# Kernel tuning notes

Hardware: AMD Instinct MI355X
Metric: run time of the kernel (lower is better)

## Reference

```python
import jax, jax.numpy as jnp
import numpy as np

B, S, H, F, E, TOPK = 4, 2048, 1024, 4096, 8, 2

def setup_inputs() -> dict:
    key = jax.random.key(0)
    ks = jax.random.split(key, 8)
    sh = 1.0 / np.sqrt(H)
    sf = 1.0 / np.sqrt(F)
    return {
        "hidden_states": jax.random.normal(ks[0], (B, S, H), jnp.float32),
        "Wr": jax.random.normal(ks[1], (H, E), jnp.float32) * sh,
        "br": jnp.zeros((E,), jnp.float32),
        "W1": jax.random.normal(ks[2], (E, H, F), jnp.float32) * sh,
        "b1": jax.random.normal(ks[3], (E, F), jnp.float32) * 0.01,
        "W2": jax.random.normal(ks[4], (E, F, H), jnp.float32) * sf,
        "b2": jax.random.normal(ks[5], (E, H), jnp.float32) * 0.01,
    }

def reference(hidden_states, Wr, br, W1, b1, W2, b2):
    b, s, h = hidden_states.shape
    x = hidden_states.reshape(-1, h)                      # [T, H]
    T = x.shape[0]
    logits = x @ Wr + br                                  # [T, E]
    routing_weights = jax.nn.softmax(logits, axis=-1)     # [T, E]
    top_v, top_i = jax.lax.top_k(logits, TOPK)            # [T, k]
    top_gates = jax.nn.softmax(top_v, axis=-1)            # [T, k]
    rows = jnp.arange(T)[:, None]
    dispatch = jnp.zeros((T, E), logits.dtype).at[rows, top_i].set(top_gates)  # [T, E]
    # Each expert runs densely on gate-scaled tokens: gelu((g*x)@W1 + b1)@W2 + b2.
    # (g*x)@W1 == g * (x@W1), so share the first GEMM across experts.
    z = jnp.einsum('th,ehf->etf', x, W1)                  # [E, T, F]
    a = jax.nn.gelu(dispatch.T[:, :, None] * z + b1[:, None, :], approximate=False)
    expert_out = jnp.einsum('etf,efh->eth', a, W2) + b2[:, None, :]  # [E, T, H]
    combined = jnp.einsum('te,eth->th', dispatch, expert_out)        # [T, H]
    final_output = combined.reshape(b, s, h)
    aux_loss = jnp.sum(routing_weights.mean(axis=0) * (dispatch.sum(axis=0) / T)) * E
    return (final_output,
            routing_weights.reshape(b, s, E),
            dispatch.reshape(b, s, E),
            aux_loss,
            logits.reshape(b, s, E))
```

## Files before the change

kernel.cpp:

```cpp
#include <hip/hip_runtime.h>

#define T_TOK 8192
#define H_DIM 1024
#define F_DIM 4096
#define E_NUM 8

typedef __attribute__((ext_vector_type(8))) short short8;
typedef __attribute__((ext_vector_type(4))) float f32x4;

__device__ __forceinline__ unsigned short f2bf(float f) {
  unsigned int u = __float_as_uint(f);
  return (unsigned short)((u + 0x7fffu + ((u >> 16) & 1u)) >> 16);
}

__device__ __forceinline__ void gload16(const void* g, void* l) {
  __builtin_amdgcn_global_load_lds(
      (__attribute__((address_space(1))) const unsigned int*)(unsigned long long)g,
      (__attribute__((address_space(3))) unsigned int*)(unsigned int)(unsigned long long)l,
      16, 0, 0);
}

__global__ __launch_bounds__(256) void k_convert_x(const float* __restrict__ x,
                                                   unsigned short* __restrict__ xb) {
  int i = blockIdx.x * blockDim.x + threadIdx.x;
  float4 v = ((const float4*)x)[i];
  unsigned int lo = (unsigned int)f2bf(v.x) | ((unsigned int)f2bf(v.y) << 16);
  unsigned int hi = (unsigned int)f2bf(v.z) | ((unsigned int)f2bf(v.w) << 16);
  ((uint2*)xb)[i] = make_uint2(lo, hi);
}

__global__ __launch_bounds__(256) void k_transpose_cvt(const float* __restrict__ in,
                                                       unsigned short* __restrict__ out,
                                                       int R, int C) {
  __shared__ float tile[32][33];
  const size_t eoff = (size_t)blockIdx.z * R * C;
  const int c0 = blockIdx.x * 32, r0 = blockIdx.y * 32;
  const int tx = threadIdx.x & 31, ty = threadIdx.x >> 5;
#pragma unroll
  for (int i = 0; i < 32; i += 8)
    tile[ty + i][tx] = in[eoff + (size_t)(r0 + ty + i) * C + (c0 + tx)];
  __syncthreads();
#pragma unroll
  for (int i = 0; i < 32; i += 8)
    out[eoff + (size_t)(c0 + ty + i) * R + (r0 + tx)] = f2bf(tile[tx][ty + i]);
}

__global__ __launch_bounds__(256) void k_logits(const float* __restrict__ x,
                                                const float* __restrict__ Wr,
                                                const float* __restrict__ br,
                                                double* __restrict__ ld,
                                                float* __restrict__ out_logits) {
  const int lane = threadIdx.x & 63;
  const int t = blockIdx.x * 4 + (threadIdx.x >> 6);
  double acc[8] = {0, 0, 0, 0, 0, 0, 0, 0};
#pragma unroll
  for (int i = 0; i < 16; ++i) {
    const int h = i * 64 + lane;
    const float xv = x[(size_t)t * H_DIM + h];
    const float4 wa = ((const float4*)Wr)[h * 2];
    const float4 wb = ((const float4*)Wr)[h * 2 + 1];
    acc[0] += (double)xv * wa.x; acc[1] += (double)xv * wa.y;
    acc[2] += (double)xv * wa.z; acc[3] += (double)xv * wa.w;
    acc[4] += (double)xv * wb.x; acc[5] += (double)xv * wb.y;
    acc[6] += (double)xv * wb.z; acc[7] += (double)xv * wb.w;
  }
#pragma unroll
  for (int e = 0; e < 8; ++e)
#pragma unroll
    for (int m = 32; m; m >>= 1) acc[e] += __shfl_xor(acc[e], m);
  if (lane == 0) {
#pragma unroll
    for (int e = 0; e < 8; ++e) {
      const double l = acc[e] + (double)br[e];
      ld[(size_t)t * 8 + e] = l;
      out_logits[(size_t)t * 8 + e] = (float)l;
    }
  }
}

__global__ __launch_bounds__(256) void k_decide(const double* __restrict__ ld,
                                                float* __restrict__ out_rw,
                                                float* __restrict__ out_disp,
                                                int* __restrict__ cnt,
                                                int* __restrict__ bidx,
                                                float* __restrict__ bgate,
                                                float* __restrict__ sums) {
  __shared__ int hcnt[8];
  __shared__ int hbase[8];
  __shared__ float srw[8];
  __shared__ float sds[8];
  const int tloc = threadIdx.x;
  const int t = blockIdx.x * 256 + tloc;
  const int lane = tloc & 63;
  if (tloc < 8) { hcnt[tloc] = 0; srw[tloc] = 0.0f; sds[tloc] = 0.0f; }
  __syncthreads();

  double l[8];
#pragma unroll
  for (int e = 0; e < 8; ++e) l[e] = ld[(size_t)t * 8 + e];
  double mx = l[0];
#pragma unroll
  for (int e = 1; e < 8; ++e) mx = l[e] > mx ? l[e] : mx;
  double ex[8], se = 0.0;
#pragma unroll
  for (int e = 0; e < 8; ++e) { ex[e] = exp(l[e] - mx); se += ex[e]; }
  int i1 = 0;
#pragma unroll
  for (int e = 1; e < 8; ++e) if (l[e] > l[i1]) i1 = e;
  int i2 = (i1 == 0) ? 1 : 0;
#pragma unroll
  for (int e = 0; e < 8; ++e) if (e != i1 && l[e] > l[i2]) i2 = e;
  const double g1 = 1.0 / (1.0 + exp(l[i2] - l[i1]));
  const double g2 = 1.0 - g1;

  float rwv[8];
#pragma unroll
  for (int e = 0; e < 8; ++e) {
    rwv[e] = (float)(ex[e] / se);
    out_rw[(size_t)t * 8 + e] = rwv[e];
    out_disp[(size_t)t * 8 + e] = (e == i1) ? (float)g1 : (e == i2) ? (float)g2 : 0.0f;
  }
#pragma unroll
  for (int e = 0; e < 8; ++e) {
    float v = rwv[e];
#pragma unroll
    for (int m = 32; m; m >>= 1) v += __shfl_xor(v, m);
    if (lane == 0) atomicAdd(&srw[e], v);
  }
  atomicAdd(&sds[i1], (float)g1);
  atomicAdd(&sds[i2], (float)g2);

  const int loc1 = atomicAdd(&hcnt[i1], 1);
  const int loc2 = atomicAdd(&hcnt[i2], 1);
  __syncthreads();
  if (tloc < 8) hbase[tloc] = atomicAdd(&cnt[tloc], hcnt[tloc]);
  __syncthreads();
  const int s1 = hbase[i1] + loc1;
  const int s2 = hbase[i2] + loc2;
  bidx[i1 * T_TOK + s1] = t; bgate[i1 * T_TOK + s1] = (float)g1;
  bidx[i2 * T_TOK + s2] = t; bgate[i2 * T_TOK + s2] = (float)g2;
  if (tloc < 8) {
    atomicAdd(&sums[tloc], srw[tloc]);
    atomicAdd(&sums[8 + tloc], sds[tloc]);
  }
}

__global__ void k_prefix_aux(const int* __restrict__ cnt, int* __restrict__ abase,
                             const float* __restrict__ sums, float* __restrict__ out_aux) {
  if (threadIdx.x == 0) {
    int base = 0;
    for (int e = 0; e < 8; ++e) { abase[e] = base; base += (cnt[e] + 127) & ~127; }
    abase[8] = base;
    double aux = 0.0;
    for (int e = 0; e < 8; ++e) aux += ((double)sums[e] / 8192.0) * ((double)sums[8 + e] / 8192.0);
    *out_aux = (float)(aux * 8.0);
  }
}


#define MFMA_Q(qm_, qn_, Bset_)                                                        \
  do {                                                                                 \
    _Pragma("unroll") for (int kh = 0; kh < 2; ++kh)                                   \
    _Pragma("unroll") for (int mi = 0; mi < 4; ++mi)                                   \
    _Pragma("unroll") for (int ni = 0; ni < 2; ++ni)                                   \
      acc[(qm_)*4 + mi][(qn_)*2 + ni] = __builtin_amdgcn_mfma_f32_16x16x32_bf16(       \
          Areg[mi][kh], Bset_[ni][kh], acc[(qm_)*4 + mi][(qn_)*2 + ni], 0, 0, 0);      \
  } while (0)

#define LOAD_A(mh_)                                                                    \
  do {                                                                                 \
    const char* Ab = smem + slot * 65536 + (mh_)*16384;                                \
    _Pragma("unroll") for (int mi = 0; mi < 4; ++mi) {                                 \
      Areg[mi][0] = *(const short8*)(Ab + mi * 2048 + aoffk0);                         \
      Areg[mi][1] = *(const short8*)(Ab + mi * 2048 + aoffk1);                         \
    }                                                                                  \
  } while (0)

#define LOAD_B(set_, nh_)                                                              \
  do {                                                                                 \
    const char* Bb = smem + slot * 65536 + 32768 + (nh_)*16384;                        \
    _Pragma("unroll") for (int ni = 0; ni < 2; ++ni) {                                 \
      set_[ni][0] = *(const short8*)(Bb + ni * 2048 + boffk0);                         \
      set_[ni][1] = *(const short8*)(Bb + ni * 2048 + boffk1);                         \
    }                                                                                  \
  } while (0)

#define PHASE_TAIL(MFMA_STMT)                                                          \
  __builtin_amdgcn_s_barrier();                                                        \
  __builtin_amdgcn_s_setprio(1);                                                       \
  MFMA_STMT;                                                                           \
  __builtin_amdgcn_s_setprio(0);                                                       \
  __builtin_amdgcn_s_barrier();

__global__ __launch_bounds__(512, 2) void k_gemm1(
    const unsigned short* __restrict__ xb, const unsigned short* __restrict__ w1t,
    const float* __restrict__ b1, const int* __restrict__ bidx,
    const float* __restrict__ bgate, const int* __restrict__ abase,
    unsigned short* __restrict__ abuf) {
  constexpr int NT = 16;
  const int e = blockIdx.z, by = blockIdx.y, bx = blockIdx.x;
  const int pb = abase[e], pcnt = abase[e + 1] - pb;
  if (by * 256 >= pcnt) return;
  __shared__ char smem[131072];
  const int tid = threadIdx.x, wid = tid >> 6, lane = tid & 63;
  const int wr = wid >> 2, wc = wid & 3;
  const int rr0 = tid >> 3;
  const int kbyte = ((tid & 7) ^ (rr0 & 7)) * 16;
  const int d0 = tid * 16, d1 = d0 + 8192;

  const int* bidx_e = bidx + e * T_TOK + by * 256;
  int tok[4];
#pragma unroll
  for (int i = 0; i < 4; ++i) tok[i] = bidx_e[i * 64 + rr0];

  const int brB0 = ((rr0 >> 5) * 64 + (rr0 & 31));
  const char* Bbase = (const char*)(w1t + (size_t)e * F_DIM * H_DIM + (size_t)(bx * 256) * H_DIM);

#define G1_STAGE_A(g_, mh_)                                                            \
  do {                                                                                 \
    const char* s0 = (const char*)(xb + (size_t)tok[(mh_)] * H_DIM) + (g_)*128 + kbyte;\
    const char* s1 = (const char*)(xb + (size_t)tok[2 + (mh_)] * H_DIM) + (g_)*128 + kbyte; \
    char* dst = smem + (((g_)&1) * 65536) + (mh_)*16384;                               \
    gload16(s0, dst + d0); gload16(s1, dst + d1);                                      \
  } while (0)

#define G1_STAGE_B(g_, nh_)                                                            \
  do {                                                                                 \
    const char* s0 = Bbase + (size_t)(brB0 + (nh_)*32) * 2048 + (g_)*128 + kbyte;      \
    const char* s1 = Bbase + (size_t)(brB0 + 128 + (nh_)*32) * 2048 + (g_)*128 + kbyte;\
    char* dst = smem + (((g_)&1) * 65536) + 32768 + (nh_)*16384;                       \
    gload16(s0, dst + d0); gload16(s1, dst + d1);                                      \
  } while (0)

  const int aoffk0 = (wr * 64 + (lane & 15)) * 128 + (((lane >> 4) ^ (lane & 7)) * 16);
  const int aoffk1 = aoffk0 ^ 64;
  const int boffk0 = (wc * 32 + (lane & 15)) * 128 + (((lane >> 4) ^ (lane & 7)) * 16);
  const int boffk1 = boffk0 ^ 64;

  f32x4 acc[8][4] = {};
  short8 Areg[4][2], B0reg[2][2], B1reg[2][2];

  G1_STAGE_A(0, 0); G1_STAGE_B(0, 1); G1_STAGE_A(0, 1); G1_STAGE_B(0, 0);
  G1_STAGE_A(1, 0); G1_STAGE_B(1, 1); G1_STAGE_A(1, 1);
  asm volatile("s_waitcnt vmcnt(6)" ::: "memory");
  __builtin_amdgcn_sched_barrier(0);
  __builtin_amdgcn_s_barrier();

  for (int g = 0; g < NT; ++g) {
    const int slot = g & 1;
    LOAD_A(0); LOAD_B(B0reg, 0);
    if (g + 1 < NT) G1_STAGE_B(g + 1, 0);
    PHASE_TAIL(MFMA_Q(0, 0, B0reg));
    LOAD_B(B1reg, 1);
    if (g + 2 < NT) G1_STAGE_A(g + 2, 0);
    PHASE_TAIL(MFMA_Q(0, 1, B1reg));
    LOAD_A(1);
    if (g + 2 < NT) G1_STAGE_B(g + 2, 1);
    PHASE_TAIL(MFMA_Q(1, 1, B1reg));
    if (g + 2 < NT) {
      G1_STAGE_A(g + 2, 1);
      asm volatile("s_waitcnt vmcnt(6)" ::: "memory");
    } else if (g + 1 < NT) {
      asm volatile("s_waitcnt vmcnt(0)" ::: "memory");
    }
    __builtin_amdgcn_sched_barrier(0);
    PHASE_TAIL(MFMA_Q(1, 0, B0reg));
  }

  const int lcol = lane & 15;
  const int gcol0 = bx * 256 + wc * 64;
  float b1v[4];
#pragma unroll
  for (int n = 0; n < 4; ++n) b1v[n] = b1[(size_t)e * F_DIM + gcol0 + n * 16 + lcol];
  const float* bg_e = bgate + e * T_TOK + by * 256;
#pragma unroll
  for (int m = 0; m < 8; ++m) {
    const int rl = wr * 128 + m * 16 + (lane >> 4) * 4;
#pragma unroll
    for (int j = 0; j < 4; ++j) {
      const int row = rl + j;
      if (by * 256 + row < pcnt) {
        const float gt = bg_e[row];
        unsigned short* orow = abuf + (size_t)(pb + by * 256 + row) * F_DIM + gcol0;
#pragma unroll
        for (int n = 0; n < 4; ++n) {
          const float v = fmaf(gt, acc[m][n][j], b1v[n]);
          const float a = 0.5f * v * (1.0f + erff(v * 0.70710678118654752f));
          orow[n * 16 + lcol] = f2bf(a);
        }
      }
    }
  }
#undef G1_STAGE_A
#undef G1_STAGE_B
}

__global__ __launch_bounds__(512, 2) void k_gemm2(
    const unsigned short* __restrict__ abuf, const unsigned short* __restrict__ w2t,
    const float* __restrict__ b2, const int* __restrict__ bidx,
    const float* __restrict__ bgate, const int* __restrict__ abase,
    const int* __restrict__ cnt, float* __restrict__ out) {
  constexpr int NT = 64;
  const int e = blockIdx.z, by = blockIdx.y, bx = blockIdx.x;
  const int pb = abase[e], pcnt = abase[e + 1] - pb;
  if (by * 256 >= pcnt) return;
  const int ce = cnt[e];
  __shared__ char smem[131072];
  const int tid = threadIdx.x, wid = tid >> 6, lane = tid & 63;
  const int wr = wid >> 2, wc = wid & 3;
  const int rr0 = tid >> 3;
  const int kbyte = ((tid & 7) ^ (rr0 & 7)) * 16;
  const int d0 = tid * 16, d1 = d0 + 8192;

  const char* Abase = (const char*)(abuf + (size_t)(pb + by * 256) * F_DIM);
  const int brB0 = ((rr0 >> 5) * 64 + (rr0 & 31));
  const char* Bbase = (const char*)(w2t + (size_t)e * H_DIM * F_DIM + (size_t)(bx * 256) * F_DIM);

#define G2_STAGE_A(g_, mh_)                                                            \
  do {                                                                                 \
    const char* s0 = Abase + (size_t)((mh_)*64 + rr0) * 8192 + (g_)*128 + kbyte;       \
    const char* s1 = Abase + (size_t)(128 + (mh_)*64 + rr0) * 8192 + (g_)*128 + kbyte; \
    char* dst = smem + (((g_)&1) * 65536) + (mh_)*16384;                               \
    gload16(s0, dst + d0); gload16(s1, dst + d1);                                      \
  } while (0)

#define G2_STAGE_B(g_, nh_)                                                            \
  do {                                                                                 \
    const char* s0 = Bbase + (size_t)(brB0 + (nh_)*32) * 8192 + (g_)*128 + kbyte;      \
    const char* s1 = Bbase + (size_t)(brB0 + 128 + (nh_)*32) * 8192 + (g_)*128 + kbyte;\
    char* dst = smem + (((g_)&1) * 65536) + 32768 + (nh_)*16384;                       \
    gload16(s0, dst + d0); gload16(s1, dst + d1);                                      \
  } while (0)

  const int aoffk0 = (wr * 64 + (lane & 15)) * 128 + (((lane >> 4) ^ (lane & 7)) * 16);
  const int aoffk1 = aoffk0 ^ 64;
  const int boffk0 = (wc * 32 + (lane & 15)) * 128 + (((lane >> 4) ^ (lane & 7)) * 16);
  const int boffk1 = boffk0 ^ 64;

  f32x4 acc[8][4] = {};
  short8 Areg[4][2], B0reg[2][2], B1reg[2][2];

  G2_STAGE_A(0, 0); G2_STAGE_B(0, 1); G2_STAGE_A(0, 1); G2_STAGE_B(0, 0);
  G2_STAGE_A(1, 0); G2_STAGE_B(1, 1); G2_STAGE_A(1, 1);
  asm volatile("s_waitcnt vmcnt(6)" ::: "memory");
  __builtin_amdgcn_sched_barrier(0);
  __builtin_amdgcn_s_barrier();

  for (int g = 0; g < NT; ++g) {
    const int slot = g & 1;
    LOAD_A(0); LOAD_B(B0reg, 0);
    if (g + 1 < NT) G2_STAGE_B(g + 1, 0);
    PHASE_TAIL(MFMA_Q(0, 0, B0reg));
    LOAD_B(B1reg, 1);
    if (g + 2 < NT) G2_STAGE_A(g + 2, 0);
    PHASE_TAIL(MFMA_Q(0, 1, B1reg));
    LOAD_A(1);
    if (g + 2 < NT) G2_STAGE_B(g + 2, 1);
    PHASE_TAIL(MFMA_Q(1, 1, B1reg));
    if (g + 2 < NT) {
      G2_STAGE_A(g + 2, 1);
      asm volatile("s_waitcnt vmcnt(6)" ::: "memory");
    } else if (g + 1 < NT) {
      asm volatile("s_waitcnt vmcnt(0)" ::: "memory");
    }
    __builtin_amdgcn_sched_barrier(0);
    PHASE_TAIL(MFMA_Q(1, 0, B0reg));
  }

  const int lcol = lane & 15;
  const int gcol0 = bx * 256 + wc * 64;
  float b2v[4];
#pragma unroll
  for (int n = 0; n < 4; ++n) b2v[n] = b2[(size_t)e * H_DIM + gcol0 + n * 16 + lcol];
  const float* bg_e = bgate + e * T_TOK;
  const int* bi_e = bidx + e * T_TOK;
#pragma unroll
  for (int m = 0; m < 8; ++m) {
    const int rl = wr * 128 + m * 16 + (lane >> 4) * 4;
#pragma unroll
    for (int j = 0; j < 4; ++j) {
      const int gm = by * 256 + rl + j;
      if (gm < ce) {
        const float gt = bg_e[gm];
        float* orow = out + (size_t)bi_e[gm] * H_DIM + gcol0;
#pragma unroll
        for (int n = 0; n < 4; ++n)
          atomicAdd(orow + n * 16 + lcol, (acc[m][n][j] + b2v[n]) * gt);
      }
    }
  }
#undef G2_STAGE_A
#undef G2_STAGE_B
}

extern "C" void kernel_launch(void* const* d_in, const int* in_sizes, int n_in,
                              void* d_out, int out_size, void* d_ws, size_t ws_size,
                              hipStream_t stream) {
  const float* x  = (const float*)d_in[0];
  const float* Wr = (const float*)d_in[1];
  const float* br = (const float*)d_in[2];
  const float* W1 = (const float*)d_in[3];
  const float* b1 = (const float*)d_in[4];
  const float* W2 = (const float*)d_in[5];
  const float* b2 = (const float*)d_in[6];
  float* out = (float*)d_out;
  float* out_final  = out;
  float* out_rw     = out + 8388608;
  float* out_disp   = out_rw + 65536;
  float* out_aux    = out_disp + 65536;
  float* out_logits = out_aux + 1;

  char* ws = (char*)d_ws;
  unsigned short* xb   = (unsigned short*)(ws);
  unsigned short* w1t  = (unsigned short*)(ws + 16777216);
  unsigned short* w2t  = (unsigned short*)(ws + 83886080);
  unsigned short* abuf = (unsigned short*)(ws + 150994944);
  int*    bidx  = (int*)(ws + 293601280);
  float*  bgate = (float*)(ws + 293863424);
  int*    cnt   = (int*)(ws + 294125568);
  int*    abase = (int*)(ws + 294125632);
  float*  sums  = (float*)(ws + 294125696);
  double* ld    = (double*)(ws + 294125824);

  hipMemsetAsync(cnt, 0, 64, stream);
  hipMemsetAsync(sums, 0, 64, stream);
  hipMemsetAsync(bidx, 0, 262144, stream);
  hipMemsetAsync(bgate, 0, 262144, stream);
  hipMemsetAsync(out_final, 0, (size_t)8388608 * 4, stream);

  k_convert_x<<<8192, 256, 0, stream>>>(x, xb);
  k_transpose_cvt<<<dim3(128, 32, 8), 256, 0, stream>>>(W1, w1t, H_DIM, F_DIM);
  k_transpose_cvt<<<dim3(32, 128, 8), 256, 0, stream>>>(W2, w2t, F_DIM, H_DIM);
  k_logits<<<2048, 256, 0, stream>>>(x, Wr, br, ld, out_logits);
  k_decide<<<32, 256, 0, stream>>>(ld, out_rw, out_disp, cnt, bidx, bgate, sums);
  k_prefix_aux<<<1, 64, 0, stream>>>(cnt, abase, sums, out_aux);
  k_gemm1<<<dim3(16, 32, 8), 512, 0, stream>>>(xb, w1t, b1, bidx, bgate, abase, abuf);
  k_gemm2<<<dim3(4, 32, 8), 512, 0, stream>>>(abuf, w2t, b2, bidx, bgate, abase, cnt, out_final);
}
```

Before: 607.2 us.

## Make expert GEMMs persistent with compact tile queues, split-K, and LDS-staged stores

The prefix kernel now builds per-expert tile offsets into a device-global queue. Both grouped GEMMs launch a fixed grid of 256 persistent blocks that walk that compact tile list, instead of a 3D grid where most blocks exit early. GEMM2 also splits K in two, relying on the existing atomic adds, so there are more tiles to balance across CUs. GEMM1's epilogue stages results through swizzled LDS so it can issue 16-byte coalesced stores in place of scattered 2-byte writes. The trade-offs are extra __syncthreads per tile, twice the atomic traffic in GEMM2, and possible load imbalance from the static stride over tiles.

```diff
diff --git a/kernel.cpp b/kernel.cpp
--- a/kernel.cpp
+++ b/kernel.cpp
@@ -7,6 +7,8 @@
 
 typedef __attribute__((ext_vector_type(8))) short short8;
 typedef __attribute__((ext_vector_type(4))) float f32x4;
+
+__device__ int g_tq[32];
 
 __device__ __forceinline__ unsigned short f2bf(float f) {
   unsigned int u = __float_as_uint(f);
@@ -148,9 +150,18 @@
 __global__ void k_prefix_aux(const int* __restrict__ cnt, int* __restrict__ abase,
                              const float* __restrict__ sums, float* __restrict__ out_aux) {
   if (threadIdx.x == 0) {
-    int base = 0;
-    for (int e = 0; e < 8; ++e) { abase[e] = base; base += (cnt[e] + 127) & ~127; }
+    int base = 0, t1 = 0, t2 = 0;
+    for (int e = 0; e < 8; ++e) {
+      abase[e] = base;
+      const int pc = (cnt[e] + 127) & ~127;
+      base += pc;
+      const int nby = (pc + 255) >> 8;
+      g_tq[e] = t1;      t1 += nby * 16;
+      g_tq[16 + e] = t2; t2 += nby * 8;
+    }
     abase[8] = base;
+    g_tq[8] = t1;
+    g_tq[24] = t2;
     double aux = 0.0;
     for (int e = 0; e < 8; ++e) aux += ((double)sums[e] / 8192.0) * ((double)sums[8 + e] / 8192.0);
     *out_aux = (float)(aux * 8.0);
@@ -198,23 +209,33 @@
     const float* __restrict__ bgate, const int* __restrict__ abase,
     unsigned short* __restrict__ abuf) {
   constexpr int NT = 16;
-  const int e = blockIdx.z, by = blockIdx.y, bx = blockIdx.x;
-  const int pb = abase[e], pcnt = abase[e + 1] - pb;
-  if (by * 256 >= pcnt) return;
   __shared__ char smem[131072];
   const int tid = threadIdx.x, wid = tid >> 6, lane = tid & 63;
   const int wr = wid >> 2, wc = wid & 3;
   const int rr0 = tid >> 3;
   const int kbyte = ((tid & 7) ^ (rr0 & 7)) * 16;
   const int d0 = tid * 16, d1 = d0 + 8192;
-
-  const int* bidx_e = bidx + e * T_TOK + by * 256;
-  int tok[4];
-#pragma unroll
-  for (int i = 0; i < 4; ++i) tok[i] = bidx_e[i * 64 + rr0];
-
-  const int brB0 = ((rr0 >> 5) * 64 + (rr0 & 31));
-  const char* Bbase = (const char*)(w1t + (size_t)e * F_DIM * H_DIM + (size_t)(bx * 256) * H_DIM);
+  const int aoffk0 = (wr * 64 + (lane & 15)) * 128 + (((lane >> 4) ^ (lane & 7)) * 16);
+  const int aoffk1 = aoffk0 ^ 64;
+  const int boffk0 = (wc * 32 + (lane & 15)) * 128 + (((lane >> 4) ^ (lane & 7)) * 16);
+  const int boffk1 = boffk0 ^ 64;
+  const int lcol = lane & 15;
+  const int total = g_tq[8];
+
+  for (int tix = blockIdx.x; tix < total; tix += gridDim.x) {
+    int e = 0;
+#pragma unroll
+    for (int q = 1; q < 8; ++q) if (g_tq[q] <= tix) e = q;
+    const int local = tix - g_tq[e];
+    const int by = local >> 4, bx = local & 15;
+    const int pb = abase[e], pcnt = abase[e + 1] - pb;
+
+    const int* bidx_e = bidx + e * T_TOK + by * 256;
+    int tok[4];
+#pragma unroll
+    for (int i = 0; i < 4; ++i) tok[i] = bidx_e[i * 64 + rr0];
+    const int brB0 = ((rr0 >> 5) * 64 + (rr0 & 31));
+    const char* Bbase = (const char*)(w1t + (size_t)e * F_DIM * H_DIM + (size_t)(bx * 256) * H_DIM);
 
 #define G1_STAGE_A(g_, mh_)                                                            \
   do {                                                                                 \
@@ -232,67 +253,74 @@
     gload16(s0, dst + d0); gload16(s1, dst + d1);                                      \
   } while (0)
 
-  const int aoffk0 = (wr * 64 + (lane & 15)) * 128 + (((lane >> 4) ^ (lane & 7)) * 16);
-  const int aoffk1 = aoffk0 ^ 64;
-  const int boffk0 = (wc * 32 + (lane & 15)) * 128 + (((lane >> 4) ^ (lane & 7)) * 16);
-  const int boffk1 = boffk0 ^ 64;
-
-  f32x4 acc[8][4] = {};
-  short8 Areg[4][2], B0reg[2][2], B1reg[2][2];
-
-  G1_STAGE_A(0, 0); G1_STAGE_B(0, 1); G1_STAGE_A(0, 1); G1_STAGE_B(0, 0);
-  G1_STAGE_A(1, 0); G1_STAGE_B(1, 1); G1_STAGE_A(1, 1);
-  asm volatile("s_waitcnt vmcnt(6)" ::: "memory");
-  __builtin_amdgcn_sched_barrier(0);
-  __builtin_amdgcn_s_barrier();
-
-  for (int g = 0; g < NT; ++g) {
-    const int slot = g & 1;
-    LOAD_A(0); LOAD_B(B0reg, 0);
-    if (g + 1 < NT) G1_STAGE_B(g + 1, 0);
-    PHASE_TAIL(MFMA_Q(0, 0, B0reg));
-    LOAD_B(B1reg, 1);
-    if (g + 2 < NT) G1_STAGE_A(g + 2, 0);
-    PHASE_TAIL(MFMA_Q(0, 1, B1reg));
-    LOAD_A(1);
-    if (g + 2 < NT) G1_STAGE_B(g + 2, 1);
-    PHASE_TAIL(MFMA_Q(1, 1, B1reg));
-    if (g + 2 < NT) {
-      G1_STAGE_A(g + 2, 1);
-      asm volatile("s_waitcnt vmcnt(6)" ::: "memory");
-    } else if (g + 1 < NT) {
-      asm volatile("s_waitcnt vmcnt(0)" ::: "memory");
-    }
+    f32x4 acc[8][4] = {};
+    short8 Areg[4][2], B0reg[2][2], B1reg[2][2];
+
+    __syncthreads();
+    G1_STAGE_A(0, 0); G1_STAGE_B(0, 1); G1_STAGE_A(0, 1); G1_STAGE_B(0, 0);
+    G1_STAGE_A(1, 0); G1_STAGE_B(1, 1); G1_STAGE_A(1, 1);
+    asm volatile("s_waitcnt vmcnt(6)" ::: "memory");
     __builtin_amdgcn_sched_barrier(0);
-    PHASE_TAIL(MFMA_Q(1, 0, B0reg));
-  }
-
-  const int lcol = lane & 15;
-  const int gcol0 = bx * 256 + wc * 64;
-  float b1v[4];
-#pragma unroll
-  for (int n = 0; n < 4; ++n) b1v[n] = b1[(size_t)e * F_DIM + gcol0 + n * 16 + lcol];
-  const float* bg_e = bgate + e * T_TOK + by * 256;
-#pragma unroll
-  for (int m = 0; m < 8; ++m) {
-    const int rl = wr * 128 + m * 16 + (lane >> 4) * 4;
-#pragma unroll
-    for (int j = 0; j < 4; ++j) {
-      const int row = rl + j;
-      if (by * 256 + row < pcnt) {
-        const float gt = bg_e[row];
-        unsigned short* orow = abuf + (size_t)(pb + by * 256 + row) * F_DIM + gcol0;
+    __builtin_amdgcn_s_barrier();
+
+    for (int g = 0; g < NT; ++g) {
+      const int slot = g & 1;
+      LOAD_A(0); LOAD_B(B0reg, 0);
+      if (g + 1 < NT) G1_STAGE_B(g + 1, 0);
+      PHASE_TAIL(MFMA_Q(0, 0, B0reg));
+      LOAD_B(B1reg, 1);
+      if (g + 2 < NT) G1_STAGE_A(g + 2, 0);
+      PHASE_TAIL(MFMA_Q(0, 1, B1reg));
+      LOAD_A(1);
+      if (g + 2 < NT) G1_STAGE_B(g + 2, 1);
+      PHASE_TAIL(MFMA_Q(1, 1, B1reg));
+      if (g + 2 < NT) {
+        G1_STAGE_A(g + 2, 1);
+        asm volatile("s_waitcnt vmcnt(6)" ::: "memory");
+      } else if (g + 1 < NT) {
+        asm volatile("s_waitcnt vmcnt(0)" ::: "memory");
+      }
+      __builtin_amdgcn_sched_barrier(0);
+      PHASE_TAIL(MFMA_Q(1, 0, B0reg));
+    }
+
+    const int gcol0 = bx * 256 + wc * 64;
+    float b1v[4];
+#pragma unroll
+    for (int n = 0; n < 4; ++n) b1v[n] = b1[(size_t)e * F_DIM + gcol0 + n * 16 + lcol];
+    const float* bg_e = bgate + e * T_TOK + by * 256;
+    char* wsm = smem + wid * 16384;
+#pragma unroll
+    for (int m = 0; m < 8; ++m) {
+      const int rbase = m * 16 + (lane >> 4) * 4;
+#pragma unroll
+      for (int j = 0; j < 4; ++j) {
+        const int wrow = rbase + j;
+        const int trow = wr * 128 + wrow;
+        const float gt = (by * 256 + trow < pcnt) ? bg_e[trow] : 0.0f;
 #pragma unroll
         for (int n = 0; n < 4; ++n) {
           const float v = fmaf(gt, acc[m][n][j], b1v[n]);
           const float a = 0.5f * v * (1.0f + erff(v * 0.70710678118654752f));
-          orow[n * 16 + lcol] = f2bf(a);
+          const int col2 = (n * 16 + lcol) * 2;
+          *(unsigned short*)(wsm + wrow * 128 + (col2 ^ ((wrow & 7) << 4))) = f2bf(a);
         }
       }
     }
-  }
+    __syncthreads();
+#pragma unroll
+    for (int r = 0; r < 16; ++r) {
+      const int row = r * 8 + (lane >> 3);
+      const int chunk = (lane & 7) ^ (row & 7);
+      const int trow = wr * 128 + row;
+      if (by * 256 + trow < pcnt) {
+        short8 vv = *(const short8*)(wsm + row * 128 + chunk * 16);
+        *(short8*)(abuf + (size_t)(pb + by * 256 + trow) * F_DIM + bx * 256 + wc * 64 + (lane & 7) * 8) = vv;
+      }
+    }
 #undef G1_STAGE_A
 #undef G1_STAGE_B
+  }
 }
 
 __global__ __launch_bounds__(512, 2) void k_gemm2(
@@ -300,21 +328,33 @@
     const float* __restrict__ b2, const int* __restrict__ bidx,
     const float* __restrict__ bgate, const int* __restrict__ abase,
     const int* __restrict__ cnt, float* __restrict__ out) {
-  constexpr int NT = 64;
-  const int e = blockIdx.z, by = blockIdx.y, bx = blockIdx.x;
-  const int pb = abase[e], pcnt = abase[e + 1] - pb;
-  if (by * 256 >= pcnt) return;
-  const int ce = cnt[e];
+  constexpr int NTH = 32;
   __shared__ char smem[131072];
   const int tid = threadIdx.x, wid = tid >> 6, lane = tid & 63;
   const int wr = wid >> 2, wc = wid & 3;
   const int rr0 = tid >> 3;
   const int kbyte = ((tid & 7) ^ (rr0 & 7)) * 16;
   const int d0 = tid * 16, d1 = d0 + 8192;
-
-  const char* Abase = (const char*)(abuf + (size_t)(pb + by * 256) * F_DIM);
-  const int brB0 = ((rr0 >> 5) * 64 + (rr0 & 31));
-  const char* Bbase = (const char*)(w2t + (size_t)e * H_DIM * F_DIM + (size_t)(bx * 256) * F_DIM);
+  const int aoffk0 = (wr * 64 + (lane & 15)) * 128 + (((lane >> 4) ^ (lane & 7)) * 16);
+  const int aoffk1 = aoffk0 ^ 64;
+  const int boffk0 = (wc * 32 + (lane & 15)) * 128 + (((lane >> 4) ^ (lane & 7)) * 16);
+  const int boffk1 = boffk0 ^ 64;
+  const int lcol = lane & 15;
+  const int total = g_tq[24];
+
+  for (int tix = blockIdx.x; tix < total; tix += gridDim.x) {
+    int e = 0;
+#pragma unroll
+    for (int q = 1; q < 8; ++q) if (g_tq[16 + q] <= tix) e = q;
+    const int local = tix - g_tq[16 + e];
+    const int by = local >> 3, bx = (local >> 1) & 3, ks = local & 1;
+    const int pb = abase[e], pcnt = abase[e + 1] - pb;
+    const int ce = cnt[e];
+    const int g0 = ks * NTH, g1 = g0 + NTH;
+
+    const char* Abase = (const char*)(abuf + (size_t)(pb + by * 256) * F_DIM);
+    const int brB0 = ((rr0 >> 5) * 64 + (rr0 & 31));
+    const char* Bbase = (const char*)(w2t + (size_t)e * H_DIM * F_DIM + (size_t)(bx * 256) * F_DIM);
 
 #define G2_STAGE_A(g_, mh_)                                                            \
   do {                                                                                 \
@@ -332,65 +372,62 @@
     gload16(s0, dst + d0); gload16(s1, dst + d1);                                      \
   } while (0)
 
-  const int aoffk0 = (wr * 64 + (lane & 15)) * 128 + (((lane >> 4) ^ (lane & 7)) * 16);
-  const int aoffk1 = aoffk0 ^ 64;
-  const int boffk0 = (wc * 32 + (lane & 15)) * 128 + (((lane >> 4) ^ (lane & 7)) * 16);
-  const int boffk1 = boffk0 ^ 64;
-
-  f32x4 acc[8][4] = {};
-  short8 Areg[4][2], B0reg[2][2], B1reg[2][2];
-
-  G2_STAGE_A(0, 0); G2_STAGE_B(0, 1); G2_STAGE_A(0, 1); G2_STAGE_B(0, 0);
-  G2_STAGE_A(1, 0); G2_STAGE_B(1, 1); G2_STAGE_A(1, 1);
-  asm volatile("s_waitcnt vmcnt(6)" ::: "memory");
-  __builtin_amdgcn_sched_barrier(0);
-  __builtin_amdgcn_s_barrier();
-
-  for (int g = 0; g < NT; ++g) {
-    const int slot = g & 1;
-    LOAD_A(0); LOAD_B(B0reg, 0);
-    if (g + 1 < NT) G2_STAGE_B(g + 1, 0);
-    PHASE_TAIL(MFMA_Q(0, 0, B0reg));
-    LOAD_B(B1reg, 1);
-    if (g + 2 < NT) G2_STAGE_A(g + 2, 0);
-    PHASE_TAIL(MFMA_Q(0, 1, B1reg));
-    LOAD_A(1);
-    if (g + 2 < NT) G2_STAGE_B(g + 2, 1);
-    PHASE_TAIL(MFMA_Q(1, 1, B1reg));
-    if (g + 2 < NT) {
-      G2_STAGE_A(g + 2, 1);
-      asm volatile("s_waitcnt vmcnt(6)" ::: "memory");
-    } else if (g + 1 < NT) {
-      asm volatile("s_waitcnt vmcnt(0)" ::: "memory");
-    }
+    f32x4 acc[8][4] = {};
+    short8 Areg[4][2], B0reg[2][2], B1reg[2][2];
+
+    __syncthreads();
+    G2_STAGE_A(g0, 0); G2_STAGE_B(g0, 1); G2_STAGE_A(g0, 1); G2_STAGE_B(g0, 0);
+    G2_STAGE_A(g0 + 1, 0); G2_STAGE_B(g0 + 1, 1); G2_STAGE_A(g0 + 1, 1);
+    asm volatile("s_waitcnt vmcnt(6)" ::: "memory");
     __builtin_amdgcn_sched_barrier(0);
-    PHASE_TAIL(MFMA_Q(1, 0, B0reg));
-  }
-
-  const int lcol = lane & 15;
-  const int gcol0 = bx * 256 + wc * 64;
-  float b2v[4];
-#pragma unroll
-  for (int n = 0; n < 4; ++n) b2v[n] = b2[(size_t)e * H_DIM + gcol0 + n * 16 + lcol];
-  const float* bg_e = bgate + e * T_TOK;
-  const int* bi_e = bidx + e * T_TOK;
-#pragma unroll
-  for (int m = 0; m < 8; ++m) {
-    const int rl = wr * 128 + m * 16 + (lane >> 4) * 4;
-#pragma unroll
-    for (int j = 0; j < 4; ++j) {
-      const int gm = by * 256 + rl + j;
-      if (gm < ce) {
-        const float gt = bg_e[gm];
-        float* orow = out + (size_t)bi_e[gm] * H_DIM + gcol0;
-#pragma unroll
-        for (int n = 0; n < 4; ++n)
-          atomicAdd(orow + n * 16 + lcol, (acc[m][n][j] + b2v[n]) * gt);
+    __builtin_amdgcn_s_barrier();
+
+    for (int g = g0; g < g1; ++g) {
+      const int slot = g & 1;
+      LOAD_A(0); LOAD_B(B0reg, 0);
+      if (g + 1 < g1) G2_STAGE_B(g + 1, 0);
+      PHASE_TAIL(MFMA_Q(0, 0, B0reg));
+      LOAD_B(B1reg, 1);
+      if (g + 2 < g1) G2_STAGE_A(g + 2, 0);
+      PHASE_TAIL(MFMA_Q(0, 1, B1reg));
+      LOAD_A(1);
+      if (g + 2 < g1) G2_STAGE_B(g + 2, 1);
+      PHASE_TAIL(MFMA_Q(1, 1, B1reg));
+      if (g + 2 < g1) {
+        G2_STAGE_A(g + 2, 1);
+        asm volatile("s_waitcnt vmcnt(6)" ::: "memory");
+      } else if (g + 1 < g1) {
+        asm volatile("s_waitcnt vmcnt(0)" ::: "memory");
       }
-    }
-  }
+      __builtin_amdgcn_sched_barrier(0);
+      PHASE_TAIL(MFMA_Q(1, 0, B0reg));
+    }
+
+    const int gcol0 = bx * 256 + wc * 64;
+    float b2v[4];
+#pragma unroll
+    for (int n = 0; n < 4; ++n)
+      b2v[n] = ks ? 0.0f : b2[(size_t)e * H_DIM + gcol0 + n * 16 + lcol];
+    const float* bg_e = bgate + e * T_TOK;
+    const int* bi_e = bidx + e * T_TOK;
+#pragma unroll
+    for (int m = 0; m < 8; ++m) {
+      const int rl = wr * 128 + m * 16 + (lane >> 4) * 4;
+#pragma unroll
+      for (int j = 0; j < 4; ++j) {
+        const int gm = by * 256 + rl + j;
+        if (gm < ce) {
+          const float gt = bg_e[gm];
+          float* orow = out + (size_t)bi_e[gm] * H_DIM + gcol0;
+#pragma unroll
+          for (int n = 0; n < 4; ++n)
+            atomicAdd(orow + n * 16 + lcol, (acc[m][n][j] + b2v[n]) * gt);
+        }
+      }
+    }
 #undef G2_STAGE_A
 #undef G2_STAGE_B
+  }
 }
 
 extern "C" void kernel_launch(void* const* d_in, const int* in_sizes, int n_in,
@@ -434,6 +471,6 @@
   k_logits<<<2048, 256, 0, stream>>>(x, Wr, br, ld, out_logits);
   k_decide<<<32, 256, 0, stream>>>(ld, out_rw, out_disp, cnt, bidx, bgate, sums);
   k_prefix_aux<<<1, 64, 0, stream>>>(cnt, abase, sums, out_aux);
-  k_gemm1<<<dim3(16, 32, 8), 512, 0, stream>>>(xb, w1t, b1, bidx, bgate, abase, abuf);
-  k_gemm2<<<dim3(4, 32, 8), 512, 0, stream>>>(abuf, w2t, b2, bidx, bgate, abase, cnt, out_final);
-}
+  k_gemm1<<<256, 512, 0, stream>>>(xb, w1t, b1, bidx, bgate, abase, abuf);
+  k_gemm2<<<256, 512, 0, stream>>>(abuf, w2t, b2, bidx, bgate, abase, cnt, out_final);
+}
```

New measurement: 846.7 us. +39.4%, slower.

## Replace atomic scatter-add with per-slot expert output plus combine kernel

Applied to the files above, without the earlier changes.

GEMM2 now writes gated expert rows into a packed per-slot buffer with plain stores. A new combine kernel gathers each token's two rows via a slot map recorded in the decide kernel. This removes the fp32 atomicAdd scatter and the memset of the final output. GEMM1's epilogue now stages GELU output through swizzled LDS so it can write 16-byte coalesced rows, and the weight transpose uses 64-row tiles with 64-wide output stores. The cost is an extra round trip through a 64MB intermediate buffer and one more launch; the buffer reuses the xb/w1t workspace after GEMM1 has finished with them.

```diff
diff --git a/kernel.cpp b/kernel.cpp
--- a/kernel.cpp
+++ b/kernel.cpp
@@ -32,17 +32,18 @@
 __global__ __launch_bounds__(256) void k_transpose_cvt(const float* __restrict__ in,
                                                        unsigned short* __restrict__ out,
                                                        int R, int C) {
-  __shared__ float tile[32][33];
+  __shared__ float tile[64][33];
   const size_t eoff = (size_t)blockIdx.z * R * C;
-  const int c0 = blockIdx.x * 32, r0 = blockIdx.y * 32;
+  const int c0 = blockIdx.x * 32, r0 = blockIdx.y * 64;
   const int tx = threadIdx.x & 31, ty = threadIdx.x >> 5;
 #pragma unroll
-  for (int i = 0; i < 32; i += 8)
-    tile[ty + i][tx] = in[eoff + (size_t)(r0 + ty + i) * C + (c0 + tx)];
+  for (int i = 0; i < 8; ++i)
+    tile[ty + i * 8][tx] = in[eoff + (size_t)(r0 + ty + i * 8) * C + (c0 + tx)];
   __syncthreads();
-#pragma unroll
-  for (int i = 0; i < 32; i += 8)
-    out[eoff + (size_t)(c0 + ty + i) * R + (r0 + tx)] = f2bf(tile[tx][ty + i]);
+  const int ow = threadIdx.x & 63, oc = threadIdx.x >> 6;
+#pragma unroll
+  for (int i = 0; i < 8; ++i)
+    out[eoff + (size_t)(c0 + oc + i * 4) * R + (r0 + ow)] = f2bf(tile[ow][oc + i * 4]);
 }
 
 __global__ __launch_bounds__(256) void k_logits(const float* __restrict__ x,
@@ -84,7 +85,8 @@
                                                 int* __restrict__ cnt,
                                                 int* __restrict__ bidx,
                                                 float* __restrict__ bgate,
-                                                float* __restrict__ sums) {
+                                                float* __restrict__ sums,
+                                                int* __restrict__ slotmap) {
   __shared__ int hcnt[8];
   __shared__ int hbase[8];
   __shared__ float srw[8];
@@ -139,6 +141,8 @@
   const int s2 = hbase[i2] + loc2;
   bidx[i1 * T_TOK + s1] = t; bgate[i1 * T_TOK + s1] = (float)g1;
   bidx[i2 * T_TOK + s2] = t; bgate[i2 * T_TOK + s2] = (float)g2;
+  slotmap[t * 2]     = (i1 << 16) | s1;
+  slotmap[t * 2 + 1] = (i2 << 16) | s2;
   if (tloc < 8) {
     atomicAdd(&sums[tloc], srw[tloc]);
     atomicAdd(&sums[8 + tloc], sds[tloc]);
@@ -156,7 +160,6 @@
     *out_aux = (float)(aux * 8.0);
   }
 }
-
 
 #define MFMA_Q(qm_, qn_, Bset_)                                                        \
   do {                                                                                 \
@@ -273,22 +276,32 @@
 #pragma unroll
   for (int n = 0; n < 4; ++n) b1v[n] = b1[(size_t)e * F_DIM + gcol0 + n * 16 + lcol];
   const float* bg_e = bgate + e * T_TOK + by * 256;
+  char* wsm = smem + wid * 16384;
 #pragma unroll
   for (int m = 0; m < 8; ++m) {
-    const int rl = wr * 128 + m * 16 + (lane >> 4) * 4;
+    const int rbase = m * 16 + (lane >> 4) * 4;
 #pragma unroll
     for (int j = 0; j < 4; ++j) {
-      const int row = rl + j;
-      if (by * 256 + row < pcnt) {
-        const float gt = bg_e[row];
-        unsigned short* orow = abuf + (size_t)(pb + by * 256 + row) * F_DIM + gcol0;
-#pragma unroll
-        for (int n = 0; n < 4; ++n) {
-          const float v = fmaf(gt, acc[m][n][j], b1v[n]);
-          const float a = 0.5f * v * (1.0f + erff(v * 0.70710678118654752f));
-          orow[n * 16 + lcol] = f2bf(a);
-        }
+      const int wrow = rbase + j;
+      const int trow = wr * 128 + wrow;
+      const float gt = (by * 256 + trow < pcnt) ? bg_e[trow] : 0.0f;
+#pragma unroll
+      for (int n = 0; n < 4; ++n) {
+        const float v = fmaf(gt, acc[m][n][j], b1v[n]);
+        const float a = 0.5f * v * (1.0f + erff(v * 0.70710678118654752f));
+        const int col2 = (n * 16 + lcol) * 2;
+        *(unsigned short*)(wsm + wrow * 128 + (col2 ^ ((wrow & 7) << 4))) = f2bf(a);
       }
+    }
+  }
+#pragma unroll
+  for (int r = 0; r < 16; ++r) {
+    const int row = r * 8 + (lane >> 3);
+    const int chunk = (lane & 7) ^ (row & 7);
+    const int trow = wr * 128 + row;
+    if (by * 256 + trow < pcnt) {
+      short8 vv = *(const short8*)(wsm + row * 128 + chunk * 16);
+      *(short8*)(abuf + (size_t)(pb + by * 256 + trow) * F_DIM + gcol0 + (lane & 7) * 8) = vv;
     }
   }
 #undef G1_STAGE_A
@@ -297,20 +310,22 @@
 
 __global__ __launch_bounds__(512, 2) void k_gemm2(
     const unsigned short* __restrict__ abuf, const unsigned short* __restrict__ w2t,
-    const float* __restrict__ b2, const int* __restrict__ bidx,
-    const float* __restrict__ bgate, const int* __restrict__ abase,
-    const int* __restrict__ cnt, float* __restrict__ out) {
+    const float* __restrict__ b2, const float* __restrict__ bgate,
+    const int* __restrict__ abase, float* __restrict__ eout) {
   constexpr int NT = 64;
   const int e = blockIdx.z, by = blockIdx.y, bx = blockIdx.x;
   const int pb = abase[e], pcnt = abase[e + 1] - pb;
   if (by * 256 >= pcnt) return;
-  const int ce = cnt[e];
   __shared__ char smem[131072];
   const int tid = threadIdx.x, wid = tid >> 6, lane = tid & 63;
   const int wr = wid >> 2, wc = wid & 3;
   const int rr0 = tid >> 3;
   const int kbyte = ((tid & 7) ^ (rr0 & 7)) * 16;
   const int d0 = tid * 16, d1 = d0 + 8192;
+  const int aoffk0 = (wr * 64 + (lane & 15)) * 128 + (((lane >> 4) ^ (lane & 7)) * 16);
+  const int aoffk1 = aoffk0 ^ 64;
+  const int boffk0 = (wc * 32 + (lane & 15)) * 128 + (((lane >> 4) ^ (lane & 7)) * 16);
+  const int boffk1 = boffk0 ^ 64;
 
   const char* Abase = (const char*)(abuf + (size_t)(pb + by * 256) * F_DIM);
   const int brB0 = ((rr0 >> 5) * 64 + (rr0 & 31));
@@ -331,11 +346,6 @@
     char* dst = smem + (((g_)&1) * 65536) + 32768 + (nh_)*16384;                       \
     gload16(s0, dst + d0); gload16(s1, dst + d1);                                      \
   } while (0)
-
-  const int aoffk0 = (wr * 64 + (lane & 15)) * 128 + (((lane >> 4) ^ (lane & 7)) * 16);
-  const int aoffk1 = aoffk0 ^ 64;
-  const int boffk0 = (wc * 32 + (lane & 15)) * 128 + (((lane >> 4) ^ (lane & 7)) * 16);
-  const int boffk1 = boffk0 ^ 64;
 
   f32x4 acc[8][4] = {};
   short8 Areg[4][2], B0reg[2][2], B1reg[2][2];
@@ -373,24 +383,37 @@
 #pragma unroll
   for (int n = 0; n < 4; ++n) b2v[n] = b2[(size_t)e * H_DIM + gcol0 + n * 16 + lcol];
   const float* bg_e = bgate + e * T_TOK;
-  const int* bi_e = bidx + e * T_TOK;
 #pragma unroll
   for (int m = 0; m < 8; ++m) {
     const int rl = wr * 128 + m * 16 + (lane >> 4) * 4;
 #pragma unroll
     for (int j = 0; j < 4; ++j) {
       const int gm = by * 256 + rl + j;
-      if (gm < ce) {
+      if (gm < pcnt) {
         const float gt = bg_e[gm];
-        float* orow = out + (size_t)bi_e[gm] * H_DIM + gcol0;
+        float* orow = eout + (size_t)(pb + gm) * H_DIM + gcol0;
 #pragma unroll
         for (int n = 0; n < 4; ++n)
-          atomicAdd(orow + n * 16 + lcol, (acc[m][n][j] + b2v[n]) * gt);
+          orow[n * 16 + lcol] = (acc[m][n][j] + b2v[n]) * gt;
       }
     }
   }
 #undef G2_STAGE_A
 #undef G2_STAGE_B
+}
+
+__global__ __launch_bounds__(256) void k_combine(const float* __restrict__ eout,
+                                                 const int* __restrict__ slotmap,
+                                                 const int* __restrict__ abase,
+                                                 float* __restrict__ outf) {
+  const int t = blockIdx.x;
+  const int c = threadIdx.x;
+  const int v0 = slotmap[t * 2], v1 = slotmap[t * 2 + 1];
+  const float* r0 = eout + (size_t)(abase[v0 >> 16] + (v0 & 0xffff)) * H_DIM;
+  const float* r1 = eout + (size_t)(abase[v1 >> 16] + (v1 & 0xffff)) * H_DIM;
+  float4 a = ((const float4*)r0)[c];
+  float4 b = ((const float4*)r1)[c];
+  ((float4*)outf)[(size_t)t * 256 + c] = make_float4(a.x + b.x, a.y + b.y, a.z + b.z, a.w + b.w);
 }
 
 extern "C" void kernel_launch(void* const* d_in, const int* in_sizes, int n_in,
@@ -421,19 +444,21 @@
   int*    abase = (int*)(ws + 294125632);
   float*  sums  = (float*)(ws + 294125696);
   double* ld    = (double*)(ws + 294125824);
+  int*    slotmap = (int*)(ws + 294650112);
+  float*  eout  = (float*)(ws);
 
   hipMemsetAsync(cnt, 0, 64, stream);
   hipMemsetAsync(sums, 0, 64, stream);
   hipMemsetAsync(bidx, 0, 262144, stream);
   hipMemsetAsync(bgate, 0, 262144, stream);
-  hipMemsetAsync(out_final, 0, (size_t)8388608 * 4, stream);
 
   k_convert_x<<<8192, 256, 0, stream>>>(x, xb);
-  k_transpose_cvt<<<dim3(128, 32, 8), 256, 0, stream>>>(W1, w1t, H_DIM, F_DIM);
-  k_transpose_cvt<<<dim3(32, 128, 8), 256, 0, stream>>>(W2, w2t, F_DIM, H_DIM);
+  k_transpose_cvt<<<dim3(128, 16, 8), 256, 0, stream>>>(W1, w1t, H_DIM, F_DIM);
+  k_transpose_cvt<<<dim3(32, 64, 8), 256, 0, stream>>>(W2, w2t, F_DIM, H_DIM);
   k_logits<<<2048, 256, 0, stream>>>(x, Wr, br, ld, out_logits);
-  k_decide<<<32, 256, 0, stream>>>(ld, out_rw, out_disp, cnt, bidx, bgate, sums);
+  k_decide<<<32, 256, 0, stream>>>(ld, out_rw, out_disp, cnt, bidx, bgate, sums, slotmap);
   k_prefix_aux<<<1, 64, 0, stream>>>(cnt, abase, sums, out_aux);
   k_gemm1<<<dim3(16, 32, 8), 512, 0, stream>>>(xb, w1t, b1, bidx, bgate, abase, abuf);
-  k_gemm2<<<dim3(4, 32, 8), 512, 0, stream>>>(abuf, w2t, b2, bidx, bgate, abase, cnt, out_final);
-}
+  k_gemm2<<<dim3(4, 32, 8), 512, 0, stream>>>(abuf, w2t, b2, bgate, abase, eout);
+  k_combine<<<8192, 256, 0, stream>>>(eout, slotmap, abase, out_final);
+}
```

New measurement: 580.7 us. 4.4% less time.
